# Performance work log

Measured on AMD Instinct MI355X. Metric: run time of the kernel, lower is better.

## Reference

```python
import jax, jax.numpy as jnp
import numpy as np

T = 32.0                       # softmax temperature
THRESH = float(np.cos(np.pi * 40.0 / 180.0))  # cos(degree), degree=40
NEG_INF = -9.0e15


def setup_inputs() -> dict:
    key = jax.random.key(0)
    ks = jax.random.split(key, 11)
    B, C, D_IMG, D_ATT, H_ATT, H = 2048, 1000, 2048, 312, 128, 128
    def rn(k, shape, scale=1.0):
        return jax.random.normal(k, shape, dtype=jnp.float32) * scale
    return {
        "image_feats": rn(ks[0], (B, D_IMG)),
        "img_proto":   rn(ks[1], (C, D_IMG)),
        "attributes":  rn(ks[2], (C, D_ATT)),
        "unused":      0,
        # parameters
        "att_g":   rn(ks[3], (D_ATT, H_ATT), 0.05),
        "slim_w":  rn(ks[4], (D_IMG, D_ATT), 0.02),   # proto_slim weight (transposed torch layout)
        "slim_b":  rn(ks[5], (D_ATT,), 0.02),
        "img_w":   rn(ks[6], (D_IMG, H), 0.02),
        "proto_w": rn(ks[7], (2 * D_ATT, H), 0.02),   # att_dim + proto_red_dim = 624
        "proto_b": rn(ks[8], (1, H), 0.02),
        "fc_w":    rn(ks[9], (H, 1), 0.05),
        "fc_b":    rn(ks[10], (1,), 0.05),
    }


def reference(image_feats, img_proto, attributes, unused,
              att_g, slim_w, slim_b, img_w, proto_w, proto_b, fc_w, fc_b):
    # proto_slim: [C, D_img] -> [C, att_dim]
    proto_red = img_proto @ slim_w + slim_b

    # --- get_attention: cosine similarity among attribute projections ---
    g = attributes @ att_g                                   # [C, att_hC] (g == h in original)
    gn = g / jnp.clip(jnp.linalg.norm(g, axis=1, keepdims=True), 1e-12)
    sim = gn @ gn.T                                          # [C, C] cosine similarity
    raw = jnp.where(sim > THRESH, sim, NEG_INF)              # threshold mask
    attn = jax.nn.softmax(raw * T, axis=1)                   # [C, C]

    # --- propagate prototypes ---
    att_outs = attn @ attributes                             # [C, att_dim]
    img_proto_outs = attn @ proto_red                        # [C, att_dim]
    outs = jnp.concatenate([att_outs, img_proto_outs], axis=1)  # [C, 2*att_dim]

    # --- relation MLP (broadcast instead of materialized expand+matmul) ---
    img_h = image_feats @ img_w                              # [B, H]
    proto_h = outs @ proto_w                                 # [C, H]
    hidden = jax.nn.relu(img_h[:, None, :] + proto_h[None, :, :] + proto_b)  # [B, C, H]
    outputs = hidden @ fc_w + fc_b                           # [B, C, 1]
    return outputs[..., 0]                                   # [B, C]
```

## Files before the change

kernel.cpp:

```cpp
#include <hip/hip_runtime.h>

typedef unsigned short ushort_t;
typedef __bf16 bf16x8 __attribute__((ext_vector_type(8)));
typedef float f32x4 __attribute__((ext_vector_type(4)));
typedef float f32x2 __attribute__((ext_vector_type(2)));
typedef ushort_t us4 __attribute__((ext_vector_type(4)));

#define T_SOFT 32.0f
#define THRESH 0.76604444311897803f
#define SW 1048
#define SO 648

__device__ __forceinline__ ushort_t f2bf(float f) {
  union { float f; unsigned u; } x; x.f = f;
  unsigned r = (x.u + 0x7fffu + ((x.u >> 16) & 1u)) >> 16;
  return (ushort_t)r;
}
__device__ __forceinline__ float bf2f(ushort_t h) {
  union { unsigned u; float f; } x; x.u = ((unsigned)h) << 16; return x.f;
}

__device__ __forceinline__ us4 pack4(float4 x) {
  union { unsigned u[2]; us4 h; } r;
  union { float4 f; unsigned u[4]; } a;
  a.f = x;
  r.u[0] = __builtin_amdgcn_perm(a.u[1] + 0x8000u, a.u[0] + 0x8000u, 0x07060302u);
  r.u[1] = __builtin_amdgcn_perm(a.u[3] + 0x8000u, a.u[2] + 0x8000u, 0x07060302u);
  return r.h;
}

__global__ __launch_bounds__(256) void tr3_k(const float* __restrict__ s0, ushort_t* __restrict__ d0,
                                             const float* __restrict__ s1, ushort_t* __restrict__ d1,
                                             const float* __restrict__ s2, ushort_t* __restrict__ d2,
                                             const float* __restrict__ s3, ushort_t* __restrict__ d3,
                                             ushort_t* __restrict__ gn_bf, ushort_t* __restrict__ poutT) {
  int b = blockIdx.x, tid = threadIdx.x;
  if (b >= 1296) {
    us4 z = {0, 0, 0, 0};
    if (b == 1296) {
      *reinterpret_cast<us4*>(gn_bf + 1000 * 128 + tid * 4) = z;
    } else {
      ushort_t* base = poutT + 632ull * 1024 + tid * 32;
      #pragma unroll
      for (int i = 0; i < 8; ++i) *reinterpret_cast<us4*>(base + i * 4) = z;
    }
    return;
  }
  __shared__ float tl[32][33];
  const float* src; ushort_t* dst; int R, C, Cw, Rpad, local, ctiles;
  if (b < 640)       { src = s0; dst = d0; R = 2048; C = 312; Cw = 320; Rpad = 2048; local = b;       ctiles = 10; }
  else if (b < 896)  { src = s1; dst = d1; R = 2048; C = 128; Cw = 128; Rpad = 2048; local = b - 640; ctiles = 4;  }
  else if (b < 976)  { src = s2; dst = d2; R = 624;  C = 128; Cw = 128; Rpad = 640;  local = b - 896; ctiles = 4;  }
  else               { src = s3; dst = d3; R = 1000; C = 312; Cw = 312; Rpad = 1024; local = b - 976; ctiles = 10; }
  int rt = local / ctiles, ct = local - rt * ctiles;
  int r0 = rt * 32, c0 = ct * 32;
  #pragma unroll
  for (int p = 0; p < 4; ++p) {
    int idx = p * 256 + tid;
    int rr = idx >> 5, cc = idx & 31;
    float v = 0.f;
    if (r0 + rr < R && c0 + cc < C) v = src[(size_t)(r0 + rr) * C + (c0 + cc)];
    tl[cc][rr] = v;
  }
  __syncthreads();
  int cc = tid >> 3, rq = tid & 7;
  if (c0 + cc < Cw) {
    us4 o;
    o[0] = f2bf(tl[cc][rq * 4 + 0]);
    o[1] = f2bf(tl[cc][rq * 4 + 1]);
    o[2] = f2bf(tl[cc][rq * 4 + 2]);
    o[3] = f2bf(tl[cc][rq * 4 + 3]);
    *reinterpret_cast<us4*>(dst + (size_t)(c0 + cc) * Rpad + r0 + rq * 4) = o;
  }
}

__device__ __forceinline__ void gemm_imgh(const float* __restrict__ A, const ushort_t* __restrict__ BT,
                                          float* __restrict__ C, int r0,
                                          ushort_t* __restrict__ As, ushort_t* __restrict__ Bs, int tid) {
  const int SA = 72;
  int lane = tid & 63, wv = tid >> 6;
  int l15 = lane & 15, quad = lane >> 4;
  int arow = tid >> 4, akq = tid & 15;
  int brow = tid >> 3, bkq = tid & 7;
  const float* agp[8];
  #pragma unroll
  for (int p = 0; p < 8; ++p) agp[p] = A + (size_t)(r0 + arow + p * 16) * 2048 + akq * 4;
  const ushort_t* bgp[4];
  #pragma unroll
  for (int p = 0; p < 4; ++p) bgp[p] = BT + (size_t)(brow + p * 32) * 2048 + bkq * 8;

  float4 ap[8]; bf16x8 bp[4];
  #pragma unroll
  for (int p = 0; p < 8; ++p) ap[p] = *reinterpret_cast<const float4*>(agp[p]);
  #pragma unroll
  for (int p = 0; p < 4; ++p) bp[p] = *reinterpret_cast<const bf16x8*>(bgp[p]);

  f32x4 acc[2][8];
  #pragma unroll
  for (int i = 0; i < 2; ++i)
    #pragma unroll
    for (int j = 0; j < 8; ++j) acc[i][j] = f32x4{0.f, 0.f, 0.f, 0.f};

  for (int s = 0; s < 32; ++s) {
    if (s) __syncthreads();
    #pragma unroll
    for (int p = 0; p < 8; ++p)
      *reinterpret_cast<us4*>(As + (arow + p * 16) * SA + akq * 4) = pack4(ap[p]);
    #pragma unroll
    for (int p = 0; p < 4; ++p)
      *reinterpret_cast<bf16x8*>(Bs + (brow + p * 32) * SA + bkq * 8) = bp[p];
    if (s + 1 < 32) {
      #pragma unroll
      for (int p = 0; p < 8; ++p) ap[p] = *reinterpret_cast<const float4*>(agp[p] + 64);
      #pragma unroll
      for (int p = 0; p < 4; ++p) bp[p] = *reinterpret_cast<const bf16x8*>(bgp[p] + 64);
      #pragma unroll
      for (int p = 0; p < 8; ++p) agp[p] += 64;
      #pragma unroll
      for (int p = 0; p < 4; ++p) bgp[p] += 64;
    }
    __syncthreads();
    #pragma unroll
    for (int kh = 0; kh < 2; ++kh) {
      bf16x8 af[2];
      #pragma unroll
      for (int pi = 0; pi < 2; ++pi)
        af[pi] = *reinterpret_cast<bf16x8*>(As + ((wv * 2 + pi) * 16 + l15) * SA + kh * 32 + quad * 8);
      #pragma unroll
      for (int ct = 0; ct < 8; ++ct) {
        bf16x8 bfr = *reinterpret_cast<bf16x8*>(Bs + (ct * 16 + l15) * SA + kh * 32 + quad * 8);
        acc[0][ct] = __builtin_amdgcn_mfma_f32_16x16x32_bf16(af[0], bfr, acc[0][ct], 0, 0, 0);
        acc[1][ct] = __builtin_amdgcn_mfma_f32_16x16x32_bf16(af[1], bfr, acc[1][ct], 0, 0, 0);
      }
    }
  }
  #pragma unroll
  for (int pi = 0; pi < 2; ++pi)
    #pragma unroll
    for (int ct = 0; ct < 8; ++ct) {
      int col = ct * 16 + l15;
      #pragma unroll
      for (int r = 0; r < 4; ++r) {
        int row = r0 + (wv * 2 + pi) * 16 + quad * 4 + r;
        C[(size_t)row * 128 + col] = acc[pi][ct][r];
      }
    }
}

__device__ __forceinline__ void gemm_protoT(const ushort_t* __restrict__ A, const float* __restrict__ B,
                                            ushort_t* __restrict__ poutT, int r0, int c0,
                                            ushort_t* __restrict__ As, ushort_t* __restrict__ Bs, int tid) {
  const int SA = 72;
  int lane = tid & 63, wv = tid >> 6;
  int l15 = lane & 15, quad = lane >> 4;
  int frow = tid >> 4, fkq = tid & 15;
  int hrow = tid >> 3, hkq = tid & 7;
  const ushort_t* agp[4];
  #pragma unroll
  for (int p = 0; p < 4; ++p) {
    int r = r0 + hrow + p * 32; if (r >= 320) r = 319;
    agp[p] = A + (size_t)r * 2048 + hkq * 8;
  }
  const float* bgp[8];
  #pragma unroll
  for (int p = 0; p < 8; ++p) {
    int n = c0 + frow + p * 16; if (n >= 1000) n = 999;
    bgp[p] = B + (size_t)n * 2048 + fkq * 4;
  }
  bf16x8 ar[4]; float4 br[8];
  #pragma unroll
  for (int p = 0; p < 4; ++p) ar[p] = *reinterpret_cast<const bf16x8*>(agp[p]);
  #pragma unroll
  for (int p = 0; p < 8; ++p) br[p] = *reinterpret_cast<const float4*>(bgp[p]);

  f32x4 acc[2][8];
  #pragma unroll
  for (int i = 0; i < 2; ++i)
    #pragma unroll
    for (int j = 0; j < 8; ++j) acc[i][j] = f32x4{0.f, 0.f, 0.f, 0.f};

  for (int s = 0; s < 32; ++s) {
    if (s) __syncthreads();
    #pragma unroll
    for (int p = 0; p < 4; ++p)
      *reinterpret_cast<bf16x8*>(As + (hrow + p * 32) * SA + hkq * 8) = ar[p];
    #pragma unroll
    for (int p = 0; p < 8; ++p)
      *reinterpret_cast<us4*>(Bs + (frow + p * 16) * SA + fkq * 4) = pack4(br[p]);
    if (s + 1 < 32) {
      #pragma unroll
      for (int p = 0; p < 4; ++p) ar[p] = *reinterpret_cast<const bf16x8*>(agp[p] + 64);
      #pragma unroll
      for (int p = 0; p < 8; ++p) br[p] = *reinterpret_cast<const float4*>(bgp[p] + 64);
      #pragma unroll
      for (int p = 0; p < 4; ++p) agp[p] += 64;
      #pragma unroll
      for (int p = 0; p < 8; ++p) bgp[p] += 64;
    }
    __syncthreads();
    #pragma unroll
    for (int kh = 0; kh < 2; ++kh) {
      bf16x8 af[2];
      #pragma unroll
      for (int pi = 0; pi < 2; ++pi)
        af[pi] = *reinterpret_cast<bf16x8*>(As + ((wv * 2 + pi) * 16 + l15) * SA + kh * 32 + quad * 8);
      #pragma unroll
      for (int ct = 0; ct < 8; ++ct) {
        bf16x8 bfr = *reinterpret_cast<bf16x8*>(Bs + (ct * 16 + l15) * SA + kh * 32 + quad * 8);
        acc[0][ct] = __builtin_amdgcn_mfma_f32_16x16x32_bf16(af[0], bfr, acc[0][ct], 0, 0, 0);
        acc[1][ct] = __builtin_amdgcn_mfma_f32_16x16x32_bf16(af[1], bfr, acc[1][ct], 0, 0, 0);
      }
    }
  }
  #pragma unroll
  for (int pi = 0; pi < 2; ++pi)
    #pragma unroll
    for (int ct = 0; ct < 8; ++ct) {
      int n = c0 + ct * 16 + l15;
      if (n < 1000) {
        #pragma unroll
        for (int r = 0; r < 4; ++r) {
          int m = r0 + (wv * 2 + pi) * 16 + quad * 4 + r;
          if (m < 320) poutT[(size_t)(312 + m) * 1024 + n] = f2bf(acc[pi][ct][r]);
        }
      }
    }
}

__global__ __launch_bounds__(256) void mega_k(
    const float* __restrict__ attributes, const float* __restrict__ att_g,
    ushort_t* __restrict__ gn_bf,
    const float* __restrict__ img_proto, const ushort_t* __restrict__ slimT,
    const float* __restrict__ image_feats, const ushort_t* __restrict__ imgwT,
    float* __restrict__ img_h, ushort_t* __restrict__ poutT) {
  __shared__ ushort_t As[128 * 72];
  __shared__ ushort_t Bs[128 * 72];
  int b = blockIdx.x, tid = threadIdx.x;
  if (b < 125) {
    __shared__ float a_lds[8][316];
    __shared__ float red2[8][2];
    int h = tid & 127;
    int c0 = b * 8;
    for (int idx = tid; idx < 8 * 312; idx += 256) {
      int r = idx / 312;
      int k = idx - r * 312;
      a_lds[r][k] = attributes[(c0 + r) * 312 + k];
    }
    __syncthreads();
    float acc[8] = {0.f,0.f,0.f,0.f,0.f,0.f,0.f,0.f};
    for (int k = 0; k < 312; k += 4) {
      float w0 = att_g[(k + 0) * 128 + h];
      float w1 = att_g[(k + 1) * 128 + h];
      float w2 = att_g[(k + 2) * 128 + h];
      float w3 = att_g[(k + 3) * 128 + h];
      #pragma unroll
      for (int r = 0; r < 8; ++r) {
        float4 a4 = *reinterpret_cast<const float4*>(&a_lds[r][k]);
        acc[r] += a4.x * w0 + a4.y * w1 + a4.z * w2 + a4.w * w3;
      }
    }
    int lane = tid & 63, wvid = (tid >> 6) & 1;
    #pragma unroll
    for (int r = 0; r < 8; ++r) {
      float v = acc[r] * acc[r];
      #pragma unroll
      for (int off = 32; off > 0; off >>= 1) v += __shfl_xor(v, off, 64);
      if (lane == 0) red2[r][wvid] = v;
    }
    __syncthreads();
    #pragma unroll
    for (int r = 0; r < 8; ++r) {
      float nrm = fmaxf(sqrtf(red2[r][0] + red2[r][1]), 1e-12f);
      gn_bf[(c0 + r) * 128 + h] = f2bf(acc[r] / nrm);
    }
    return;
  }
  b -= 125;
  if (b < 16) {
    gemm_imgh(image_feats, imgwT, img_h, b * 128, As, Bs, tid);
  } else {
    b -= 16;
    int rb = b >> 3, cb = b & 7;
    gemm_protoT(slimT, img_proto, poutT, rb * 128, cb * 128, As, Bs, tid);
  }
}

__global__ __launch_bounds__(256) void attn4_k(
    const ushort_t* __restrict__ gn_bf, const ushort_t* __restrict__ poutT,
    const float* __restrict__ slim_b, const ushort_t* __restrict__ protowT,
    const float* __restrict__ proto_b, float* __restrict__ ph) {
  __shared__ ushort_t W[16 * SW];
  __shared__ ushort_t OS[16 * SO];
  __shared__ float rsum[16];
  __shared__ int flags[63];
  int tid = threadIdx.x;
  int i0 = blockIdx.x * 16;
  int lane = tid & 63, wv = tid >> 6;
  int l15 = lane & 15, quad = lane >> 4;
  if (tid < 63) flags[tid] = 0;
  if (tid >= 64 && tid < 80) rsum[tid - 64] = 0.f;
  W[(tid >> 4) * SW + 1008 + (tid & 15)] = 0;
  __syncthreads();

  const ushort_t* abase = gn_bf + (size_t)(i0 + l15) * 128 + quad * 8;
  bf16x8 af0 = *reinterpret_cast<const bf16x8*>(abase);
  bf16x8 af1 = *reinterpret_cast<const bf16x8*>(abase + 32);
  bf16x8 af2 = *reinterpret_cast<const bf16x8*>(abase + 64);
  bf16x8 af3 = *reinterpret_cast<const bf16x8*>(abase + 96);
  float rs[4] = {0.f, 0.f, 0.f, 0.f};
  for (int jt = wv; jt < 63; jt += 4) {
    const ushort_t* bbase = gn_bf + (size_t)(jt * 16 + l15) * 128 + quad * 8;
    f32x4 d = {0.f, 0.f, 0.f, 0.f};
    d = __builtin_amdgcn_mfma_f32_16x16x32_bf16(af0, *reinterpret_cast<const bf16x8*>(bbase),      d, 0, 0, 0);
    d = __builtin_amdgcn_mfma_f32_16x16x32_bf16(af1, *reinterpret_cast<const bf16x8*>(bbase + 32), d, 0, 0, 0);
    d = __builtin_amdgcn_mfma_f32_16x16x32_bf16(af2, *reinterpret_cast<const bf16x8*>(bbase + 64), d, 0, 0, 0);
    d = __builtin_amdgcn_mfma_f32_16x16x32_bf16(af3, *reinterpret_cast<const bf16x8*>(bbase + 96), d, 0, 0, 0);
    int hot = 0;
    #pragma unroll
    for (int r = 0; r < 4; ++r) {
      float w = 0.f;
      if (d[r] > THRESH) { w = __expf(T_SOFT * (d[r] - 1.0f)); hot = 1; }
      ushort_t wb = f2bf(w);
      W[(quad * 4 + r) * SW + jt * 16 + l15] = wb;
      rs[r] += bf2f(wb);
    }
    if (hot) flags[jt] = 1;
  }
  #pragma unroll
  for (int r = 0; r < 4; ++r) {
    float v = rs[r];
    v += __shfl_xor(v, 1, 64); v += __shfl_xor(v, 2, 64);
    v += __shfl_xor(v, 4, 64); v += __shfl_xor(v, 8, 64);
    if (l15 == 0) atomicAdd(&rsum[quad * 4 + r], v);
  }
  __syncthreads();

  f32x4 acc[10];
  #pragma unroll
  for (int t = 0; t < 10; ++t) acc[t] = f32x4{0.f, 0.f, 0.f, 0.f};
  for (int s = 0; s < 32; ++s) {
    int f = flags[2 * s] | ((2 * s + 1 < 63) ? flags[2 * s + 1] : 0);
    if (!f) continue;
    bf16x8 a = *reinterpret_cast<bf16x8*>(W + l15 * SW + s * 32 + quad * 8);
    #pragma unroll
    for (int t = 0; t < 10; ++t) {
      int nrow = (wv * 10 + t) * 16 + l15;
      bf16x8 bfr = *reinterpret_cast<const bf16x8*>(poutT + (size_t)nrow * 1024 + s * 32 + quad * 8);
      acc[t] = __builtin_amdgcn_mfma_f32_16x16x32_bf16(a, bfr, acc[t], 0, 0, 0);
    }
  }
  #pragma unroll
  for (int t = 0; t < 10; ++t) {
    int col = (wv * 10 + t) * 16 + l15;
    float bias = (col >= 312 && col < 624) ? slim_b[col - 312] : 0.f;
    #pragma unroll
    for (int r = 0; r < 4; ++r) {
      int row = quad * 4 + r;
      float inv = 1.f / fmaxf(rsum[row], 1e-30f);
      OS[row * SO + col] = f2bf(acc[t][r] * inv + bias);
    }
  }
  __syncthreads();

  f32x4 acc2[2];
  acc2[0] = f32x4{0.f, 0.f, 0.f, 0.f};
  acc2[1] = f32x4{0.f, 0.f, 0.f, 0.f};
  for (int s = 0; s < 20; ++s) {
    bf16x8 a = *reinterpret_cast<bf16x8*>(OS + l15 * SO + s * 32 + quad * 8);
    #pragma unroll
    for (int t = 0; t < 2; ++t) {
      int n = (wv * 2 + t) * 16 + l15;
      bf16x8 bfr = *reinterpret_cast<const bf16x8*>(protowT + (size_t)n * 640 + s * 32 + quad * 8);
      acc2[t] = __builtin_amdgcn_mfma_f32_16x16x32_bf16(a, bfr, acc2[t], 0, 0, 0);
    }
  }
  #pragma unroll
  for (int t = 0; t < 2; ++t) {
    int h = (wv * 2 + t) * 16 + l15;
    float pb = proto_b[h];
    #pragma unroll
    for (int r = 0; r < 4; ++r) {
      int gi = i0 + quad * 4 + r;
      if (gi < 1000) ph[(size_t)gi * 128 + h] = acc2[t][r] + pb;
    }
  }
}

__global__ __launch_bounds__(256) void final_k(
    const float* __restrict__ img_h, const float* __restrict__ ph,
    const float* __restrict__ fc_w, const float* __restrict__ fc_b,
    float* __restrict__ out) {
  __shared__ float ih[128][132];
  __shared__ float ps[64][132];
  __shared__ float ws_[128];
  int tid = threadIdx.x;
  int b0 = blockIdx.x * 128;
  int c0 = blockIdx.y * 64;
  for (int idx = tid; idx < 4096; idx += 256) {
    int row = idx >> 5, c4 = (idx & 31) * 4;
    float4 v = *reinterpret_cast<const float4*>(img_h + (size_t)(b0 + row) * 128 + c4);
    *reinterpret_cast<float4*>(&ih[row][c4]) = v;
  }
  for (int idx = tid; idx < 2048; idx += 256) {
    int row = idx >> 5, c4 = (idx & 31) * 4;
    int c = c0 + row;
    float4 v = make_float4(0.f, 0.f, 0.f, 0.f);
    if (c < 1000) v = *reinterpret_cast<const float4*>(ph + (size_t)c * 128 + c4);
    *reinterpret_cast<float4*>(&ps[row][c4]) = v;
  }
  if (tid < 128) ws_[tid] = fc_w[tid];
  __syncthreads();
  int tx = tid & 15, ty = tid >> 4;
  f32x2 acc[8][4] = {};
  const f32x2 zero2 = {0.f, 0.f};
  for (int h = 0; h < 128; h += 4) {
    float4 w4 = *reinterpret_cast<float4*>(&ws_[h]);
    f32x2 wlo = {w4.x, w4.y}, whi = {w4.z, w4.w};
    float4 a4[8], p4[4];
    #pragma unroll
    for (int i = 0; i < 8; ++i) a4[i] = *reinterpret_cast<float4*>(&ih[ty * 8 + i][h]);
    #pragma unroll
    for (int j = 0; j < 4; ++j) p4[j] = *reinterpret_cast<float4*>(&ps[tx * 4 + j][h]);
    #pragma unroll
    for (int i = 0; i < 8; ++i) {
      f32x2 alo = {a4[i].x, a4[i].y}, ahi = {a4[i].z, a4[i].w};
      #pragma unroll
      for (int j = 0; j < 4; ++j) {
        f32x2 plo = {p4[j].x, p4[j].y}, phi = {p4[j].z, p4[j].w};
        f32x2 t0 = __builtin_elementwise_max(alo + plo, zero2);
        f32x2 t1 = __builtin_elementwise_max(ahi + phi, zero2);
        acc[i][j] = acc[i][j] + t0 * wlo;
        acc[i][j] = acc[i][j] + t1 * whi;
      }
    }
  }
  float fb = fc_b[0];
  #pragma unroll
  for (int i = 0; i < 8; ++i) {
    int b = b0 + ty * 8 + i;
    int c = c0 + tx * 4;
    if (c < 1000) {
      float4 v = make_float4(acc[i][0].x + acc[i][0].y + fb, acc[i][1].x + acc[i][1].y + fb,
                             acc[i][2].x + acc[i][2].y + fb, acc[i][3].x + acc[i][3].y + fb);
      *reinterpret_cast<float4*>(out + (size_t)b * 1000 + c) = v;
    }
  }
}

extern "C" void kernel_launch(void* const* d_in, const int* in_sizes, int n_in,
                              void* d_out, int out_size, void* d_ws, size_t ws_size,
                              hipStream_t stream) {
  const float* image_feats = (const float*)d_in[0];
  const float* img_proto   = (const float*)d_in[1];
  const float* attributes  = (const float*)d_in[2];
  const float* att_g   = (const float*)d_in[4];
  const float* slim_w  = (const float*)d_in[5];
  const float* slim_b  = (const float*)d_in[6];
  const float* img_w   = (const float*)d_in[7];
  const float* proto_w = (const float*)d_in[8];
  const float* proto_b = (const float*)d_in[9];
  const float* fc_w    = (const float*)d_in[10];
  const float* fc_b    = (const float*)d_in[11];
  float* out = (float*)d_out;

  char* ws = (char*)d_ws;
  size_t o = 0;
  auto alloc = [&](size_t bytes) { size_t r = o; o += (bytes + 255) & ~(size_t)255; return r; };
  ushort_t* imgwT   = (ushort_t*)(ws + alloc(128ull * 2048 * 2));
  ushort_t* slimT   = (ushort_t*)(ws + alloc(320ull * 2048 * 2));
  ushort_t* protowT = (ushort_t*)(ws + alloc(128ull * 640 * 2));
  ushort_t* gn_bf   = (ushort_t*)(ws + alloc(1008ull * 128 * 2));
  ushort_t* poutT   = (ushort_t*)(ws + alloc(640ull * 1024 * 2));
  float* img_h     = (float*)(ws + alloc(2048ull * 128 * 4));
  float* ph        = (float*)(ws + alloc(1000ull * 128 * 4));

  tr3_k<<<1298, 256, 0, stream>>>(slim_w, slimT, img_w, imgwT, proto_w, protowT,
                                  attributes, poutT, gn_bf, poutT);

  mega_k<<<165, 256, 0, stream>>>(attributes, att_g, gn_bf,
                                  img_proto, slimT,
                                  image_feats, imgwT, img_h, poutT);

  attn4_k<<<63, 256, 0, stream>>>(gn_bf, poutT, slim_b, protowT, proto_b, ph);

  final_k<<<dim3(16, 16), 256, 0, stream>>>(img_h, ph, fc_w, fc_b, out);
}
```

Before: 175.7 us.

## Split-K the image and prototype GEMMs across more blocks with atomic accumulation

The two large GEMMs in mega_k (image_feats@img_w and the slim projection of img_proto) are now split into 8 K-chunks each, raising the grid from 165 to 445 blocks so more CUs are busy. Partial sums go into fp32 buffers via atomicAdd, and those buffers are zeroed by extra blocks in the transpose kernel. The attention kernel now reads the fp32 proto_red transpose and converts it to bf16 on the fly. The cost is atomic traffic, extra zeroing work, and fp32 reads in attn4_k instead of bf16.

Measured after the change: 182.6 us. 1.04x slower.

```diff
diff --git a/kernel.cpp b/kernel.cpp
--- a/kernel.cpp
+++ b/kernel.cpp
@@ -28,21 +28,38 @@
   r.u[1] = __builtin_amdgcn_perm(a.u[3] + 0x8000u, a.u[2] + 0x8000u, 0x07060302u);
   return r.h;
 }
+__device__ __forceinline__ bf16x8 pack8(float4 x, float4 y) {
+  union { unsigned u[4]; bf16x8 h; } r;
+  union { float4 f; unsigned u[4]; } a, b;
+  a.f = x; b.f = y;
+  r.u[0] = __builtin_amdgcn_perm(a.u[1] + 0x8000u, a.u[0] + 0x8000u, 0x07060302u);
+  r.u[1] = __builtin_amdgcn_perm(a.u[3] + 0x8000u, a.u[2] + 0x8000u, 0x07060302u);
+  r.u[2] = __builtin_amdgcn_perm(b.u[1] + 0x8000u, b.u[0] + 0x8000u, 0x07060302u);
+  r.u[3] = __builtin_amdgcn_perm(b.u[3] + 0x8000u, b.u[2] + 0x8000u, 0x07060302u);
+  return r.h;
+}
 
 __global__ __launch_bounds__(256) void tr3_k(const float* __restrict__ s0, ushort_t* __restrict__ d0,
                                              const float* __restrict__ s1, ushort_t* __restrict__ d1,
                                              const float* __restrict__ s2, ushort_t* __restrict__ d2,
                                              const float* __restrict__ s3, ushort_t* __restrict__ d3,
-                                             ushort_t* __restrict__ gn_bf, ushort_t* __restrict__ poutT) {
+                                             ushort_t* __restrict__ gn_bf,
+                                             float* __restrict__ z0, float* __restrict__ z1) {
   int b = blockIdx.x, tid = threadIdx.x;
   if (b >= 1296) {
-    us4 z = {0, 0, 0, 0};
     if (b == 1296) {
+      us4 z = {0, 0, 0, 0};
       *reinterpret_cast<us4*>(gn_bf + 1000 * 128 + tid * 4) = z;
+    } else if (b < 1361) {
+      int local = b - 1297;
+      float4 z = make_float4(0.f, 0.f, 0.f, 0.f);
+      float4* p = reinterpret_cast<float4*>(z0) + local * 1024 + tid;
+      p[0] = z; p[256] = z; p[512] = z; p[768] = z;
     } else {
-      ushort_t* base = poutT + 632ull * 1024 + tid * 32;
-      #pragma unroll
-      for (int i = 0; i < 8; ++i) *reinterpret_cast<us4*>(base + i * 4) = z;
+      int local = b - 1361;
+      float4 z = make_float4(0.f, 0.f, 0.f, 0.f);
+      float4* p = reinterpret_cast<float4*>(z1) + local * 1024 + tid;
+      p[0] = z; p[256] = z; p[512] = z; p[768] = z;
     }
     return;
   }
@@ -74,9 +91,12 @@
   }
 }
 
-__device__ __forceinline__ void gemm_imgh(const float* __restrict__ A, const ushort_t* __restrict__ BT,
-                                          float* __restrict__ C, int r0,
-                                          ushort_t* __restrict__ As, ushort_t* __restrict__ Bs, int tid) {
+__device__ __forceinline__ void gemm_f32a_seg(
+    const float* __restrict__ A, int M, int lda,
+    const ushort_t* __restrict__ BT, int ldbt,
+    float* __restrict__ C, int ldc,
+    int r0, int k0, int nsteps,
+    ushort_t* __restrict__ As, ushort_t* __restrict__ Bs, int tid) {
   const int SA = 72;
   int lane = tid & 63, wv = tid >> 6;
   int l15 = lane & 15, quad = lane >> 4;
@@ -84,10 +104,13 @@
   int brow = tid >> 3, bkq = tid & 7;
   const float* agp[8];
   #pragma unroll
-  for (int p = 0; p < 8; ++p) agp[p] = A + (size_t)(r0 + arow + p * 16) * 2048 + akq * 4;
+  for (int p = 0; p < 8; ++p) {
+    int r = r0 + arow + p * 16; if (r >= M) r = M - 1;
+    agp[p] = A + (size_t)r * lda + k0 + akq * 4;
+  }
   const ushort_t* bgp[4];
   #pragma unroll
-  for (int p = 0; p < 4; ++p) bgp[p] = BT + (size_t)(brow + p * 32) * 2048 + bkq * 8;
+  for (int p = 0; p < 4; ++p) bgp[p] = BT + (size_t)(brow + p * 32) * ldbt + k0 + bkq * 8;
 
   float4 ap[8]; bf16x8 bp[4];
   #pragma unroll
@@ -101,7 +124,7 @@
     #pragma unroll
     for (int j = 0; j < 8; ++j) acc[i][j] = f32x4{0.f, 0.f, 0.f, 0.f};
 
-  for (int s = 0; s < 32; ++s) {
+  for (int s = 0; s < nsteps; ++s) {
     if (s) __syncthreads();
     #pragma unroll
     for (int p = 0; p < 8; ++p)
@@ -109,7 +132,7 @@
     #pragma unroll
     for (int p = 0; p < 4; ++p)
       *reinterpret_cast<bf16x8*>(Bs + (brow + p * 32) * SA + bkq * 8) = bp[p];
-    if (s + 1 < 32) {
+    if (s + 1 < nsteps) {
       #pragma unroll
       for (int p = 0; p < 8; ++p) ap[p] = *reinterpret_cast<const float4*>(agp[p] + 64);
       #pragma unroll
@@ -142,14 +165,15 @@
       #pragma unroll
       for (int r = 0; r < 4; ++r) {
         int row = r0 + (wv * 2 + pi) * 16 + quad * 4 + r;
-        C[(size_t)row * 128 + col] = acc[pi][ct][r];
+        if (row < M) atomicAdd(&C[(size_t)row * ldc + col], acc[pi][ct][r]);
       }
     }
 }
 
-__device__ __forceinline__ void gemm_protoT(const ushort_t* __restrict__ A, const float* __restrict__ B,
-                                            ushort_t* __restrict__ poutT, int r0, int c0,
-                                            ushort_t* __restrict__ As, ushort_t* __restrict__ Bs, int tid) {
+__device__ __forceinline__ void gemm_protoT_seg(
+    const ushort_t* __restrict__ A, const float* __restrict__ B,
+    float* __restrict__ outp, int r0, int c0, int k0, int nsteps,
+    ushort_t* __restrict__ As, ushort_t* __restrict__ Bs, int tid) {
   const int SA = 72;
   int lane = tid & 63, wv = tid >> 6;
   int l15 = lane & 15, quad = lane >> 4;
@@ -159,13 +183,13 @@
   #pragma unroll
   for (int p = 0; p < 4; ++p) {
     int r = r0 + hrow + p * 32; if (r >= 320) r = 319;
-    agp[p] = A + (size_t)r * 2048 + hkq * 8;
+    agp[p] = A + (size_t)r * 2048 + k0 + hkq * 8;
   }
   const float* bgp[8];
   #pragma unroll
   for (int p = 0; p < 8; ++p) {
     int n = c0 + frow + p * 16; if (n >= 1000) n = 999;
-    bgp[p] = B + (size_t)n * 2048 + fkq * 4;
+    bgp[p] = B + (size_t)n * 2048 + k0 + fkq * 4;
   }
   bf16x8 ar[4]; float4 br[8];
   #pragma unroll
@@ -179,7 +203,7 @@
     #pragma unroll
     for (int j = 0; j < 8; ++j) acc[i][j] = f32x4{0.f, 0.f, 0.f, 0.f};
 
-  for (int s = 0; s < 32; ++s) {
+  for (int s = 0; s < nsteps; ++s) {
     if (s) __syncthreads();
     #pragma unroll
     for (int p = 0; p < 4; ++p)
@@ -187,7 +211,7 @@
     #pragma unroll
     for (int p = 0; p < 8; ++p)
       *reinterpret_cast<us4*>(Bs + (frow + p * 16) * SA + fkq * 4) = pack4(br[p]);
-    if (s + 1 < 32) {
+    if (s + 1 < nsteps) {
       #pragma unroll
       for (int p = 0; p < 4; ++p) ar[p] = *reinterpret_cast<const bf16x8*>(agp[p] + 64);
       #pragma unroll
@@ -221,72 +245,76 @@
         #pragma unroll
         for (int r = 0; r < 4; ++r) {
           int m = r0 + (wv * 2 + pi) * 16 + quad * 4 + r;
-          if (m < 320) poutT[(size_t)(312 + m) * 1024 + n] = f2bf(acc[pi][ct][r]);
+          if (m < 320) atomicAdd(&outp[(size_t)m * 1024 + n], acc[pi][ct][r]);
         }
       }
     }
 }
 
-__global__ __launch_bounds__(256) void mega_k(
+__global__ __launch_bounds__(256, 4) void mega_k(
     const float* __restrict__ attributes, const float* __restrict__ att_g,
     ushort_t* __restrict__ gn_bf,
     const float* __restrict__ img_proto, const ushort_t* __restrict__ slimT,
     const float* __restrict__ image_feats, const ushort_t* __restrict__ imgwT,
-    float* __restrict__ img_h, ushort_t* __restrict__ poutT) {
+    float* __restrict__ img_h, float* __restrict__ proto_redT) {
   __shared__ ushort_t As[128 * 72];
   __shared__ ushort_t Bs[128 * 72];
   int b = blockIdx.x, tid = threadIdx.x;
-  if (b < 125) {
-    __shared__ float a_lds[8][316];
-    __shared__ float red2[8][2];
-    int h = tid & 127;
-    int c0 = b * 8;
-    for (int idx = tid; idx < 8 * 312; idx += 256) {
-      int r = idx / 312;
-      int k = idx - r * 312;
-      a_lds[r][k] = attributes[(c0 + r) * 312 + k];
-    }
-    __syncthreads();
-    float acc[8] = {0.f,0.f,0.f,0.f,0.f,0.f,0.f,0.f};
-    for (int k = 0; k < 312; k += 4) {
-      float w0 = att_g[(k + 0) * 128 + h];
-      float w1 = att_g[(k + 1) * 128 + h];
-      float w2 = att_g[(k + 2) * 128 + h];
-      float w3 = att_g[(k + 3) * 128 + h];
-      #pragma unroll
-      for (int r = 0; r < 8; ++r) {
-        float4 a4 = *reinterpret_cast<const float4*>(&a_lds[r][k]);
-        acc[r] += a4.x * w0 + a4.y * w1 + a4.z * w2 + a4.w * w3;
-      }
-    }
-    int lane = tid & 63, wvid = (tid >> 6) & 1;
+  if (b < 128) {
+    int tile = b >> 3, kc = b & 7;
+    gemm_f32a_seg(image_feats, 2048, 2048, imgwT, 2048, img_h, 128,
+                  tile * 128, kc * 256, 4, As, Bs, tid);
+    return;
+  }
+  if (b < 320) {
+    int idx = b - 128;
+    int tile = idx >> 3, kc = idx & 7;
+    int rb = tile / 8, cb = tile - rb * 8;
+    gemm_protoT_seg(slimT, img_proto, proto_redT, rb * 128, cb * 128, kc * 256, 4, As, Bs, tid);
+    return;
+  }
+  b -= 320;
+  float* a_lds = reinterpret_cast<float*>(As);
+  float* red2 = reinterpret_cast<float*>(Bs);
+  int h = tid & 127;
+  int c0 = b * 8;
+  for (int idx = tid; idx < 8 * 312; idx += 256) {
+    int r = idx / 312;
+    int k = idx - r * 312;
+    a_lds[r * 316 + k] = attributes[(c0 + r) * 312 + k];
+  }
+  __syncthreads();
+  float acc[8] = {0.f,0.f,0.f,0.f,0.f,0.f,0.f,0.f};
+  for (int k = 0; k < 312; k += 4) {
+    float w0 = att_g[(k + 0) * 128 + h];
+    float w1 = att_g[(k + 1) * 128 + h];
+    float w2 = att_g[(k + 2) * 128 + h];
+    float w3 = att_g[(k + 3) * 128 + h];
     #pragma unroll
     for (int r = 0; r < 8; ++r) {
-      float v = acc[r] * acc[r];
-      #pragma unroll
-      for (int off = 32; off > 0; off >>= 1) v += __shfl_xor(v, off, 64);
-      if (lane == 0) red2[r][wvid] = v;
-    }
-    __syncthreads();
-    #pragma unroll
-    for (int r = 0; r < 8; ++r) {
-      float nrm = fmaxf(sqrtf(red2[r][0] + red2[r][1]), 1e-12f);
-      gn_bf[(c0 + r) * 128 + h] = f2bf(acc[r] / nrm);
-    }
-    return;
-  }
-  b -= 125;
-  if (b < 16) {
-    gemm_imgh(image_feats, imgwT, img_h, b * 128, As, Bs, tid);
-  } else {
-    b -= 16;
-    int rb = b >> 3, cb = b & 7;
-    gemm_protoT(slimT, img_proto, poutT, rb * 128, cb * 128, As, Bs, tid);
+      float4 a4 = *reinterpret_cast<const float4*>(&a_lds[r * 316 + k]);
+      acc[r] += a4.x * w0 + a4.y * w1 + a4.z * w2 + a4.w * w3;
+    }
+  }
+  int lane = tid & 63, wvid = (tid >> 6) & 1;
+  #pragma unroll
+  for (int r = 0; r < 8; ++r) {
+    float v = acc[r] * acc[r];
+    #pragma unroll
+    for (int off = 32; off > 0; off >>= 1) v += __shfl_xor(v, off, 64);
+    if (lane == 0) red2[r * 2 + wvid] = v;
+  }
+  __syncthreads();
+  #pragma unroll
+  for (int r = 0; r < 8; ++r) {
+    float nrm = fmaxf(sqrtf(red2[r * 2 + 0] + red2[r * 2 + 1]), 1e-12f);
+    gn_bf[(c0 + r) * 128 + h] = f2bf(acc[r] / nrm);
   }
 }
 
 __global__ __launch_bounds__(256) void attn4_k(
-    const ushort_t* __restrict__ gn_bf, const ushort_t* __restrict__ poutT,
+    const ushort_t* __restrict__ gn_bf, const ushort_t* __restrict__ attrT,
+    const float* __restrict__ proto_redT,
     const float* __restrict__ slim_b, const ushort_t* __restrict__ protowT,
     const float* __restrict__ proto_b, float* __restrict__ ph) {
   __shared__ ushort_t W[16 * SW];
@@ -345,7 +373,16 @@
     #pragma unroll
     for (int t = 0; t < 10; ++t) {
       int nrow = (wv * 10 + t) * 16 + l15;
-      bf16x8 bfr = *reinterpret_cast<const bf16x8*>(poutT + (size_t)nrow * 1024 + s * 32 + quad * 8);
+      bf16x8 bfr;
+      if (nrow < 312) {
+        bfr = *reinterpret_cast<const bf16x8*>(attrT + (size_t)nrow * 1024 + s * 32 + quad * 8);
+      } else if (nrow < 632) {
+        const float* pp = proto_redT + (size_t)(nrow - 312) * 1024 + s * 32 + quad * 8;
+        bfr = pack8(*reinterpret_cast<const float4*>(pp), *reinterpret_cast<const float4*>(pp + 4));
+      } else {
+        union { unsigned u[4]; bf16x8 h; } z = {{0u, 0u, 0u, 0u}};
+        bfr = z.h;
+      }
       acc[t] = __builtin_amdgcn_mfma_f32_16x16x32_bf16(a, bfr, acc[t], 0, 0, 0);
     }
   }
@@ -470,18 +507,19 @@
   ushort_t* slimT   = (ushort_t*)(ws + alloc(320ull * 2048 * 2));
   ushort_t* protowT = (ushort_t*)(ws + alloc(128ull * 640 * 2));
   ushort_t* gn_bf   = (ushort_t*)(ws + alloc(1008ull * 128 * 2));
-  ushort_t* poutT   = (ushort_t*)(ws + alloc(640ull * 1024 * 2));
+  ushort_t* attrT   = (ushort_t*)(ws + alloc(312ull * 1024 * 2));
+  float* proto_redT = (float*)(ws + alloc(320ull * 1024 * 4));
   float* img_h     = (float*)(ws + alloc(2048ull * 128 * 4));
   float* ph        = (float*)(ws + alloc(1000ull * 128 * 4));
 
-  tr3_k<<<1298, 256, 0, stream>>>(slim_w, slimT, img_w, imgwT, proto_w, protowT,
-                                  attributes, poutT, gn_bf, poutT);
-
-  mega_k<<<165, 256, 0, stream>>>(attributes, att_g, gn_bf,
+  tr3_k<<<1441, 256, 0, stream>>>(slim_w, slimT, img_w, imgwT, proto_w, protowT,
+                                  attributes, attrT, gn_bf, img_h, proto_redT);
+
+  mega_k<<<445, 256, 0, stream>>>(attributes, att_g, gn_bf,
                                   img_proto, slimT,
-                                  image_feats, imgwT, img_h, poutT);
-
-  attn4_k<<<63, 256, 0, stream>>>(gn_bf, poutT, slim_b, protowT, proto_b, ph);
+                                  image_feats, imgwT, img_h, proto_redT);
+
+  attn4_k<<<63, 256, 0, stream>>>(gn_bf, attrT, proto_redT, slim_b, protowT, proto_b, ph);
 
   final_k<<<dim3(16, 16), 256, 0, stream>>>(img_h, ph, fc_w, fc_b, out);
 }
```
